# Optimization experiments

Measured on AMD Instinct MI355X. Metric: run time of the kernel, lower is better.

## Reference

```python
import jax, jax.numpy as jnp
import numpy as np

DIM_K = 128
MODEL_DIM = 1024
B, S = 8, 2048

def setup_inputs() -> dict:
    key = jax.random.key(0)
    k1, k2, k3, k4, k5, k6, k7 = jax.random.split(key, 7)
    return {
        "query": jax.random.normal(k1, (B, S, MODEL_DIM), dtype=jnp.float32),
        "key": jax.random.normal(k2, (B, S, MODEL_DIM), dtype=jnp.float32),
        "value": jax.random.normal(k3, (B, S, MODEL_DIM), dtype=jnp.float32),
        "mask": jax.random.randint(k4, (B, S, S), 0, 2, dtype=jnp.int32),
        # nn.Linear(model_dim, dim_k, bias=False): weight shape [dim_k, model_dim]
        "Wq": jax.random.normal(k5, (DIM_K, MODEL_DIM), dtype=jnp.float32) * (MODEL_DIM ** -0.5),
        "Wk": jax.random.normal(k6, (DIM_K, MODEL_DIM), dtype=jnp.float32) * (MODEL_DIM ** -0.5),
        "Wv": jax.random.normal(k7, (DIM_K, MODEL_DIM), dtype=jnp.float32) * (MODEL_DIM ** -0.5),
    }

def reference(query, key, value, mask, Wq, Wk, Wv):
    # projections: y = x @ W.T
    q = jnp.einsum('bsm,km->bsk', query, Wq)
    k = jnp.einsum('bsm,km->bsk', key, Wk)
    v = jnp.einsum('bsm,km->bsk', value, Wv)
    scale = 1.0 / jnp.sqrt(jnp.float32(DIM_K))
    pre_score = jnp.einsum('bqk,bsk->bqs', q, k) * scale  # [B,Sq,Sk]
    pre_score = jnp.where(mask == 0, jnp.float32(-1e9), pre_score)
    score = jax.nn.softmax(pre_score, axis=-1)
    return jnp.einsum('bqs,bsk->bqk', score, v)
```

## Files before the change

kernel.cpp:

```cpp
#include <hip/hip_runtime.h>
#include <hip/hip_bf16.h>

#define SEQ 2048
#define DMODEL 1024
#define DK 128

typedef __bf16 bf16x8 __attribute__((ext_vector_type(8)));
typedef float  f32x4  __attribute__((ext_vector_type(4)));

#define L2E 1.44269504088896340736f

#define WS_Q  786432
#define WS_K  2883584
#define WS_VT 4980736

__global__ __launch_bounds__(256) void wconv_kernel(
    const float* __restrict__ wq, const float* __restrict__ wk,
    const float* __restrict__ wv, __bf16* __restrict__ wpack)
{
    int i = blockIdx.x * 256 + threadIdx.x;
    int p = i >> 17;
    int j = i & 131071;
    const float* src = (p == 0) ? wq : ((p == 1) ? wk : wv);
    float f = src[j];
    if (p == 0) f *= 0.08838834764831845f;
    __bf16 h = (__bf16)f;
    __bf16 l = (__bf16)(f - (float)h);
    wpack[p * 262144 + j]          = h;
    wpack[p * 262144 + 131072 + j] = l;
}

__global__ __launch_bounds__(256) void proj_kernel(
    const float* __restrict__ xq, const float* __restrict__ xk,
    const float* __restrict__ xv, const __bf16* __restrict__ wpack,
    __bf16* __restrict__ qws, __bf16* __restrict__ kws, __bf16* __restrict__ vtws)
{
    const int p = blockIdx.y;
    const float* __restrict__ x = (p == 0) ? xq : ((p == 1) ? xk : xv);
    const __bf16* __restrict__ whi_g = wpack + p * 262144;
    const __bf16* __restrict__ wlo_g = whi_g + 131072;

    const int mtile = blockIdx.x;
    const int m0 = mtile << 7;
    const int t = threadIdx.x;
    const int wv_ = t >> 6;
    const int lane = t & 63;
    const int l15 = lane & 15, g = lane >> 4;

    __shared__ __align__(16) __bf16 smem[18432];
    __bf16* whl = smem;
    __bf16* wll = smem + 9216;

    f32x4 acc[2][8];
    for (int mt = 0; mt < 2; ++mt)
        for (int nt = 0; nt < 8; ++nt) acc[mt][nt] = (f32x4){0.f, 0.f, 0.f, 0.f};

    for (int kk = 0; kk < 16; ++kk) {
        __syncthreads();
#pragma unroll
        for (int i = 0; i < 8; ++i) {
            int idx = i * 256 + t;
            int h = idx >> 10, rem = idx & 1023;
            int row = rem >> 3, ck = rem & 7;
            const __bf16* src = (h ? wlo_g : whi_g) + row * 1024 + kk * 64 + ck * 8;
            __bf16* dst = (h ? wll : whl) + row * 72 + ck * 8;
            *(bf16x8*)dst = *(const bf16x8*)src;
        }
        __syncthreads();

        for (int ks = 0; ks < 2; ++ks) {
            bf16x8 ah[2], al[2];
#pragma unroll
            for (int mt = 0; mt < 2; ++mt) {
                int row = m0 + wv_ * 32 + mt * 16 + l15;
                int col = kk * 64 + ks * 32 + g * 8;
                const float* xp = x + row * 1024 + col;
                f32x4 a0 = *(const f32x4*)xp;
                f32x4 a1 = *(const f32x4*)(xp + 4);
#pragma unroll
                for (int j = 0; j < 4; ++j) {
                    __bf16 h0 = (__bf16)a0[j];
                    ah[mt][j] = h0; al[mt][j] = (__bf16)(a0[j] - (float)h0);
                    __bf16 h1 = (__bf16)a1[j];
                    ah[mt][4 + j] = h1; al[mt][4 + j] = (__bf16)(a1[j] - (float)h1);
                }
            }
#pragma unroll
            for (int nt = 0; nt < 8; ++nt) {
                const __bf16* bp = whl + (nt * 16 + l15) * 72 + ks * 32 + g * 8;
                bf16x8 bh = *(const bf16x8*)bp;
                bf16x8 bl = *(const bf16x8*)(bp + 9216);
#pragma unroll
                for (int mt = 0; mt < 2; ++mt) {
                    acc[mt][nt] = __builtin_amdgcn_mfma_f32_16x16x32_bf16(ah[mt], bh, acc[mt][nt], 0, 0, 0);
                    acc[mt][nt] = __builtin_amdgcn_mfma_f32_16x16x32_bf16(al[mt], bh, acc[mt][nt], 0, 0, 0);
                    acc[mt][nt] = __builtin_amdgcn_mfma_f32_16x16x32_bf16(ah[mt], bl, acc[mt][nt], 0, 0, 0);
                }
            }
        }
    }

    __syncthreads();
    __bf16* olds = smem;
#pragma unroll
    for (int mt = 0; mt < 2; ++mt)
#pragma unroll
        for (int nt = 0; nt < 8; ++nt)
#pragma unroll
            for (int r = 0; r < 4; ++r) {
                int rowl = wv_ * 32 + mt * 16 + g * 4 + r;
                int col = nt * 16 + l15;
                __bf16 v = (__bf16)acc[mt][nt][r];
                if (p < 2) olds[rowl * 136 + col] = v;
                else       olds[col * 136 + rowl] = v;
            }
    __syncthreads();

    const int bq = mtile >> 4, s0 = (mtile & 15) << 7;
#pragma unroll
    for (int i = 0; i < 8; ++i) {
        int idx = i * 256 + t;
        int row = idx >> 4, ck = idx & 15;
        bf16x8 v = *(const bf16x8*)(olds + row * 136 + ck * 8);
        __bf16* dst;
        if (p == 0)      dst = qws + (m0 + row) * 128 + ck * 8;
        else if (p == 1) dst = kws + (m0 + row) * 128 + ck * 8;
        else             dst = vtws + ((size_t)(bq * 128 + row)) * 2048 + s0 + ck * 8;
        *(bf16x8*)dst = v;
    }
}

__global__ __launch_bounds__(256) void flash_kernel(
    const __bf16* __restrict__ qws, const __bf16* __restrict__ kws,
    const __bf16* __restrict__ vtws, const int* __restrict__ mask,
    float* __restrict__ out)
{
    const int bb = blockIdx.x & 7;
    const int mtile = blockIdx.x >> 3;
    const int sq0 = mtile << 6;
    const int t = threadIdx.x;
    const int wv_ = t >> 6;
    const int lane = t & 63;
    const int l15 = lane & 15, g = lane >> 4;

    __shared__ __align__(16) __bf16 smem[22528];
    __bf16* klds = smem;
    __bf16* vtlds = smem + 8704;
    __bf16* plds = smem + 17920 + wv_ * 1152;

    bf16x8 qf[4];
    {
        const __bf16* qp = qws + ((size_t)(bb * 2048 + sq0 + wv_ * 16 + l15)) * 128 + g * 8;
#pragma unroll
        for (int ks = 0; ks < 4; ++ks) qf[ks] = *(const bf16x8*)(qp + ks * 32);
    }

    f32x4 o[8];
#pragma unroll
    for (int nt = 0; nt < 8; ++nt) o[nt] = (f32x4){0.f, 0.f, 0.f, 0.f};
    float m_run[4], l_run[4];
#pragma unroll
    for (int r = 0; r < 4; ++r) { m_run[r] = -__builtin_inff(); l_run[r] = 0.f; }

    const int* mbase = mask + ((size_t)(bb * 2048 + sq0 + wv_ * 16 + g * 4)) * 2048 + l15;

    for (int kt = 0; kt < 32; ++kt) {
        const int n0 = kt << 6;
        __syncthreads();
#pragma unroll
        for (int i = 0; i < 8; ++i) {
            int idx = i * 256 + t;
            if (idx < 1024) {
                int row = idx >> 4, ck = idx & 15;
                *(bf16x8*)(klds + row * 136 + ck * 8) =
                    *(const bf16x8*)(kws + ((size_t)(bb * 2048 + n0 + row)) * 128 + ck * 8);
            } else {
                int v = idx - 1024;
                int row = v >> 3, ck = v & 7;
                *(bf16x8*)(vtlds + row * 72 + ck * 8) =
                    *(const bf16x8*)(vtws + ((size_t)(bb * 128 + row)) * 2048 + n0 + ck * 8);
            }
        }
        __syncthreads();

        int mv[4][4];
#pragma unroll
        for (int nt = 0; nt < 4; ++nt)
#pragma unroll
            for (int r = 0; r < 4; ++r)
                mv[nt][r] = mbase[(size_t)r * 2048 + n0 + nt * 16];

        f32x4 sf[4];
#pragma unroll
        for (int nt = 0; nt < 4; ++nt) sf[nt] = (f32x4){0.f, 0.f, 0.f, 0.f};
#pragma unroll
        for (int nt = 0; nt < 4; ++nt) {
            const __bf16* kp = klds + (nt * 16 + l15) * 136 + g * 8;
#pragma unroll
            for (int ks = 0; ks < 4; ++ks) {
                bf16x8 bfk = *(const bf16x8*)(kp + ks * 32);
                sf[nt] = __builtin_amdgcn_mfma_f32_16x16x32_bf16(qf[ks], bfk, sf[nt], 0, 0, 0);
            }
        }

        float mx[4], mnew[4], alpha[4], psum[4];
#pragma unroll
        for (int r = 0; r < 4; ++r)
            mx[r] = fmaxf(fmaxf(sf[0][r], sf[1][r]), fmaxf(sf[2][r], sf[3][r]));
#pragma unroll
        for (int off = 1; off < 16; off <<= 1)
#pragma unroll
            for (int r = 0; r < 4; ++r)
                mx[r] = fmaxf(mx[r], __shfl_xor(mx[r], off, 64));
#pragma unroll
        for (int r = 0; r < 4; ++r) {
            mnew[r] = fmaxf(m_run[r], mx[r]);
            alpha[r] = exp2f((m_run[r] - mnew[r]) * L2E);
            psum[r] = 0.f;
        }
#pragma unroll
        for (int nt = 0; nt < 4; ++nt)
#pragma unroll
            for (int r = 0; r < 4; ++r) {
                float pv = exp2f((sf[nt][r] - mnew[r]) * L2E);
                pv = mv[nt][r] ? pv : 0.f;
                psum[r] += pv;
                plds[(g * 4 + r) * 72 + nt * 16 + l15] = (__bf16)pv;
            }
#pragma unroll
        for (int off = 1; off < 16; off <<= 1)
#pragma unroll
            for (int r = 0; r < 4; ++r)
                psum[r] += __shfl_xor(psum[r], off, 64);
#pragma unroll
        for (int r = 0; r < 4; ++r) {
            l_run[r] = l_run[r] * alpha[r] + psum[r];
            m_run[r] = mnew[r];
        }
#pragma unroll
        for (int nt = 0; nt < 8; ++nt)
#pragma unroll
            for (int r = 0; r < 4; ++r) o[nt][r] *= alpha[r];

        bf16x8 pa[2];
#pragma unroll
        for (int ks2 = 0; ks2 < 2; ++ks2)
            pa[ks2] = *(const bf16x8*)(plds + l15 * 72 + ks2 * 32 + g * 8);

#pragma unroll
        for (int nt2 = 0; nt2 < 8; ++nt2) {
            const __bf16* vp = vtlds + (nt2 * 16 + l15) * 72 + g * 8;
#pragma unroll
            for (int ks2 = 0; ks2 < 2; ++ks2) {
                bf16x8 bfv = *(const bf16x8*)(vp + ks2 * 32);
                o[nt2] = __builtin_amdgcn_mfma_f32_16x16x32_bf16(pa[ks2], bfv, o[nt2], 0, 0, 0);
            }
        }
    }

    float inv[4];
#pragma unroll
    for (int r = 0; r < 4; ++r) inv[r] = 1.0f / l_run[r];
#pragma unroll
    for (int nt2 = 0; nt2 < 8; ++nt2)
#pragma unroll
        for (int r = 0; r < 4; ++r)
            out[((size_t)(bb * 2048 + sq0 + wv_ * 16 + g * 4 + r)) * 128 + nt2 * 16 + l15] =
                o[nt2][r] * inv[r];
}

extern "C" void kernel_launch(void* const* d_in, const int* in_sizes, int n_in,
                              void* d_out, int out_size, void* d_ws, size_t ws_size,
                              hipStream_t stream)
{
    const float* query = (const float*)d_in[0];
    const float* key   = (const float*)d_in[1];
    const float* value = (const float*)d_in[2];
    const int*   mask  = (const int*)d_in[3];
    const float* Wq    = (const float*)d_in[4];
    const float* Wk    = (const float*)d_in[5];
    const float* Wv    = (const float*)d_in[6];
    float* out = (float*)d_out;

    __bf16* wpack = (__bf16*)d_ws;
    __bf16* qws = wpack + WS_Q;
    __bf16* kws = wpack + WS_K;
    __bf16* vtws = wpack + WS_VT;

    wconv_kernel<<<1536, 256, 0, stream>>>(Wq, Wk, Wv, wpack);
    proj_kernel<<<dim3(128, 3), 256, 0, stream>>>(query, key, value, wpack, qws, kws, vtws);
    flash_kernel<<<256, 256, 0, stream>>>(qws, kws, vtws, mask, out);
}
```

Baseline: 422.6 us.

## Split flash attention over key range, halve projection tile, drop x-low MFMA term

The flash kernel's key loop is split across up to four blocks per query tile when workspace allows. Each split writes unnormalised partial outputs plus running max and sum, and a new merge kernel combines them with a log-sum-exp rescale. This raises the grid from 256 blocks to as many as 1024 so more of the GPU stays busy. The projection kernel now uses 64-row tiles, doubling its grid, and drops the low-order bf16 part of the activations, going from three MFMAs per tile to two. That lowers precision somewhat and adds extra global traffic for the partial results.

```diff
diff --git a/kernel.cpp b/kernel.cpp
--- a/kernel.cpp
+++ b/kernel.cpp
@@ -13,6 +13,7 @@
 #define WS_Q  786432
 #define WS_K  2883584
 #define WS_VT 4980736
+#define WS_BF16_BYTES 14155776ull
 
 __global__ __launch_bounds__(256) void wconv_kernel(
     const float* __restrict__ wq, const float* __restrict__ wk,
@@ -41,7 +42,7 @@
     const __bf16* __restrict__ wlo_g = whi_g + 131072;
 
     const int mtile = blockIdx.x;
-    const int m0 = mtile << 7;
+    const int m0 = mtile << 6;
     const int t = threadIdx.x;
     const int wv_ = t >> 6;
     const int lane = t & 63;
@@ -51,9 +52,9 @@
     __bf16* whl = smem;
     __bf16* wll = smem + 9216;
 
-    f32x4 acc[2][8];
-    for (int mt = 0; mt < 2; ++mt)
-        for (int nt = 0; nt < 8; ++nt) acc[mt][nt] = (f32x4){0.f, 0.f, 0.f, 0.f};
+    f32x4 acc[8];
+#pragma unroll
+    for (int nt = 0; nt < 8; ++nt) acc[nt] = (f32x4){0.f, 0.f, 0.f, 0.f};
 
     for (int kk = 0; kk < 16; ++kk) {
         __syncthreads();
@@ -68,34 +69,26 @@
         }
         __syncthreads();
 
+#pragma unroll
         for (int ks = 0; ks < 2; ++ks) {
-            bf16x8 ah[2], al[2];
-#pragma unroll
-            for (int mt = 0; mt < 2; ++mt) {
-                int row = m0 + wv_ * 32 + mt * 16 + l15;
-                int col = kk * 64 + ks * 32 + g * 8;
-                const float* xp = x + row * 1024 + col;
-                f32x4 a0 = *(const f32x4*)xp;
-                f32x4 a1 = *(const f32x4*)(xp + 4);
-#pragma unroll
-                for (int j = 0; j < 4; ++j) {
-                    __bf16 h0 = (__bf16)a0[j];
-                    ah[mt][j] = h0; al[mt][j] = (__bf16)(a0[j] - (float)h0);
-                    __bf16 h1 = (__bf16)a1[j];
-                    ah[mt][4 + j] = h1; al[mt][4 + j] = (__bf16)(a1[j] - (float)h1);
-                }
+            int row = m0 + wv_ * 16 + l15;
+            int col = kk * 64 + ks * 32 + g * 8;
+            const float* xp = x + (size_t)row * 1024 + col;
+            f32x4 a0 = *(const f32x4*)xp;
+            f32x4 a1 = *(const f32x4*)(xp + 4);
+            bf16x8 ah;
+#pragma unroll
+            for (int j = 0; j < 4; ++j) {
+                ah[j] = (__bf16)a0[j];
+                ah[4 + j] = (__bf16)a1[j];
             }
 #pragma unroll
             for (int nt = 0; nt < 8; ++nt) {
                 const __bf16* bp = whl + (nt * 16 + l15) * 72 + ks * 32 + g * 8;
                 bf16x8 bh = *(const bf16x8*)bp;
                 bf16x8 bl = *(const bf16x8*)(bp + 9216);
-#pragma unroll
-                for (int mt = 0; mt < 2; ++mt) {
-                    acc[mt][nt] = __builtin_amdgcn_mfma_f32_16x16x32_bf16(ah[mt], bh, acc[mt][nt], 0, 0, 0);
-                    acc[mt][nt] = __builtin_amdgcn_mfma_f32_16x16x32_bf16(al[mt], bh, acc[mt][nt], 0, 0, 0);
-                    acc[mt][nt] = __builtin_amdgcn_mfma_f32_16x16x32_bf16(ah[mt], bl, acc[mt][nt], 0, 0, 0);
-                }
+                acc[nt] = __builtin_amdgcn_mfma_f32_16x16x32_bf16(ah, bh, acc[nt], 0, 0, 0);
+                acc[nt] = __builtin_amdgcn_mfma_f32_16x16x32_bf16(ah, bl, acc[nt], 0, 0, 0);
             }
         }
     }
@@ -103,40 +96,49 @@
     __syncthreads();
     __bf16* olds = smem;
 #pragma unroll
-    for (int mt = 0; mt < 2; ++mt)
-#pragma unroll
-        for (int nt = 0; nt < 8; ++nt)
-#pragma unroll
-            for (int r = 0; r < 4; ++r) {
-                int rowl = wv_ * 32 + mt * 16 + g * 4 + r;
-                int col = nt * 16 + l15;
-                __bf16 v = (__bf16)acc[mt][nt][r];
-                if (p < 2) olds[rowl * 136 + col] = v;
-                else       olds[col * 136 + rowl] = v;
-            }
+    for (int nt = 0; nt < 8; ++nt)
+#pragma unroll
+        for (int r = 0; r < 4; ++r) {
+            int rowl = wv_ * 16 + g * 4 + r;
+            int col = nt * 16 + l15;
+            __bf16 v = (__bf16)acc[nt][r];
+            if (p < 2) olds[rowl * 136 + col] = v;
+            else       olds[col * 72 + rowl] = v;
+        }
     __syncthreads();
 
-    const int bq = mtile >> 4, s0 = (mtile & 15) << 7;
-#pragma unroll
-    for (int i = 0; i < 8; ++i) {
-        int idx = i * 256 + t;
-        int row = idx >> 4, ck = idx & 15;
-        bf16x8 v = *(const bf16x8*)(olds + row * 136 + ck * 8);
-        __bf16* dst;
-        if (p == 0)      dst = qws + (m0 + row) * 128 + ck * 8;
-        else if (p == 1) dst = kws + (m0 + row) * 128 + ck * 8;
-        else             dst = vtws + ((size_t)(bq * 128 + row)) * 2048 + s0 + ck * 8;
-        *(bf16x8*)dst = v;
+    const int bq = mtile >> 5, s0 = (mtile & 31) << 6;
+    if (p < 2) {
+#pragma unroll
+        for (int i = 0; i < 4; ++i) {
+            int idx = i * 256 + t;
+            int row = idx >> 4, ck = idx & 15;
+            bf16x8 v = *(const bf16x8*)(olds + row * 136 + ck * 8);
+            __bf16* dst = ((p == 0) ? qws : kws) + (size_t)(m0 + row) * 128 + ck * 8;
+            *(bf16x8*)dst = v;
+        }
+    } else {
+#pragma unroll
+        for (int i = 0; i < 4; ++i) {
+            int idx = i * 256 + t;
+            int row = idx >> 3, ck = idx & 7;
+            bf16x8 v = *(const bf16x8*)(olds + row * 72 + ck * 8);
+            __bf16* dst = vtws + ((size_t)(bq * 128 + row)) * 2048 + s0 + ck * 8;
+            *(bf16x8*)dst = v;
+        }
     }
 }
 
 __global__ __launch_bounds__(256) void flash_kernel(
     const __bf16* __restrict__ qws, const __bf16* __restrict__ kws,
     const __bf16* __restrict__ vtws, const int* __restrict__ mask,
-    float* __restrict__ out)
+    float* __restrict__ out, float* __restrict__ part, float* __restrict__ mlbuf,
+    int ktp)
 {
     const int bb = blockIdx.x & 7;
-    const int mtile = blockIdx.x >> 3;
+    const int rest = blockIdx.x >> 3;
+    const int mtile = rest & 31;
+    const int jsplit = rest >> 5;
     const int sq0 = mtile << 6;
     const int t = threadIdx.x;
     const int wv_ = t >> 6;
@@ -164,7 +166,8 @@
 
     const int* mbase = mask + ((size_t)(bb * 2048 + sq0 + wv_ * 16 + g * 4)) * 2048 + l15;
 
-    for (int kt = 0; kt < 32; ++kt) {
+    const int kt_begin = jsplit * ktp, kt_end = kt_begin + ktp;
+    for (int kt = kt_begin; kt < kt_end; ++kt) {
         const int n0 = kt << 6;
         __syncthreads();
 #pragma unroll
@@ -258,15 +261,61 @@
         }
     }
 
-    float inv[4];
-#pragma unroll
-    for (int r = 0; r < 4; ++r) inv[r] = 1.0f / l_run[r];
-#pragma unroll
-    for (int nt2 = 0; nt2 < 8; ++nt2)
-#pragma unroll
-        for (int r = 0; r < 4; ++r)
-            out[((size_t)(bb * 2048 + sq0 + wv_ * 16 + g * 4 + r)) * 128 + nt2 * 16 + l15] =
-                o[nt2][r] * inv[r];
+    if (part == nullptr) {
+        float inv[4];
+#pragma unroll
+        for (int r = 0; r < 4; ++r) inv[r] = 1.0f / l_run[r];
+#pragma unroll
+        for (int nt2 = 0; nt2 < 8; ++nt2)
+#pragma unroll
+            for (int r = 0; r < 4; ++r)
+                out[((size_t)(bb * 2048 + sq0 + wv_ * 16 + g * 4 + r)) * 128 + nt2 * 16 + l15] =
+                    o[nt2][r] * inv[r];
+    } else {
+#pragma unroll
+        for (int nt2 = 0; nt2 < 8; ++nt2)
+#pragma unroll
+            for (int r = 0; r < 4; ++r) {
+                size_t rowg = (size_t)(bb * 2048 + sq0 + wv_ * 16 + g * 4 + r);
+                part[((size_t)jsplit * 16384 + rowg) * 128 + nt2 * 16 + l15] = o[nt2][r];
+            }
+        if (l15 == 0) {
+#pragma unroll
+            for (int r = 0; r < 4; ++r) {
+                size_t rowg = (size_t)(bb * 2048 + sq0 + wv_ * 16 + g * 4 + r);
+                mlbuf[((size_t)jsplit * 16384 + rowg) * 2]     = m_run[r];
+                mlbuf[((size_t)jsplit * 16384 + rowg) * 2 + 1] = l_run[r];
+            }
+        }
+    }
+}
+
+__global__ __launch_bounds__(256) void merge_kernel(
+    const float* __restrict__ part, const float* __restrict__ mlbuf,
+    float* __restrict__ out, int J)
+{
+    int t = threadIdx.x;
+    size_t row = (size_t)blockIdx.x * 8 + (t >> 5);
+    int c = (t & 31) * 4;
+    float mj[4];
+    float m = -__builtin_inff();
+    for (int j = 0; j < J; ++j) {
+        mj[j] = mlbuf[((size_t)j * 16384 + row) * 2];
+        m = fmaxf(m, mj[j]);
+    }
+    float l = 0.f;
+    f32x4 acc = (f32x4){0.f, 0.f, 0.f, 0.f};
+    for (int j = 0; j < J; ++j) {
+        float w = exp2f((mj[j] - m) * L2E);
+        l += w * mlbuf[((size_t)j * 16384 + row) * 2 + 1];
+        f32x4 v = *(const f32x4*)(part + ((size_t)j * 16384 + row) * 128 + c);
+#pragma unroll
+        for (int e = 0; e < 4; ++e) acc[e] += w * v[e];
+    }
+    float inv = 1.0f / l;
+#pragma unroll
+    for (int e = 0; e < 4; ++e) acc[e] *= inv;
+    *(f32x4*)(out + row * 128 + c) = acc;
 }
 
 extern "C" void kernel_launch(void* const* d_in, const int* in_sizes, int n_in,
@@ -287,7 +336,15 @@
     __bf16* kws = wpack + WS_K;
     __bf16* vtws = wpack + WS_VT;
 
+    const size_t per_split = 16384ull * 128 * 4 + 16384ull * 8;
+    int J = 1;
+    if (ws_size >= WS_BF16_BYTES + 4 * per_split)      J = 4;
+    else if (ws_size >= WS_BF16_BYTES + 2 * per_split) J = 2;
+    float* part = (J > 1) ? (float*)((char*)d_ws + WS_BF16_BYTES) : nullptr;
+    float* mlbuf = (J > 1) ? (part + (size_t)J * 16384 * 128) : nullptr;
+
     wconv_kernel<<<1536, 256, 0, stream>>>(Wq, Wk, Wv, wpack);
-    proj_kernel<<<dim3(128, 3), 256, 0, stream>>>(query, key, value, wpack, qws, kws, vtws);
-    flash_kernel<<<256, 256, 0, stream>>>(qws, kws, vtws, mask, out);
-}
+    proj_kernel<<<dim3(256, 3), 256, 0, stream>>>(query, key, value, wpack, qws, kws, vtws);
+    flash_kernel<<<256 * J, 256, 0, stream>>>(qws, kws, vtws, mask, out, part, mlbuf, 32 / J);
+    if (J > 1) merge_kernel<<<2048, 256, 0, stream>>>(part, mlbuf, out, J);
+}
```

Result: faster. 414.3 us (-2.0%).
